# Kernel tuning notes

Hardware: AMD Instinct MI355X
Metric: run time of the kernel (lower is better)

The kernel has to match this reference:

```python
import jax, jax.numpy as jnp
import numpy as np

N = 262144      # total tokens (rows of batch)
D = 256         # d_model
S = 512         # number of distinct sequence ids
MAX_LEN = 640   # static upper bound on tokens per sequence (counts ~ Binomial(N, 1/S))


def setup_inputs() -> dict:
    key = jax.random.key(0)
    k1, k2 = jax.random.split(key)
    batch = jax.random.normal(k1, (N, D), dtype=jnp.float32)
    sequence_ids = jax.random.randint(k2, (N,), 0, S, dtype=jnp.int32)
    return {"batch": batch, "sequence_ids": sequence_ids}


def reference(batch, sequence_ids):
    # Counting-sort style grouping: for each row, compute its rank within its
    # sequence-id group (preserving original order, like torch.nonzero order),
    # then scatter into a padded [S, MAX_LEN, D] tensor.
    ids = sequence_ids
    ones = jnp.ones((N,), jnp.int32)
    counts = jax.ops.segment_sum(ones, ids, num_segments=S)          # [S]
    offsets = jnp.cumsum(counts) - counts                             # start of each group in sorted order
    order = jnp.argsort(ids)                                          # stable sort by id -> original order within group
    ranks_sorted = jnp.arange(N, dtype=jnp.int32) - offsets[ids[order]]
    ranks = jnp.zeros((N,), jnp.int32).at[order].set(ranks_sorted)    # rank of each row within its group
    padded = jnp.zeros((S, MAX_LEN, D), batch.dtype).at[ids, ranks].set(batch)
    padding_mask = jnp.all(padded == 0, axis=-1)                      # [S, MAX_LEN]
    return padded, padding_mask
```

## Files before the change

kernel.cpp:

```cpp
#include <hip/hip_runtime.h>

#define N_TOK   262144
#define D       256
#define NSEQ    512
#define MAX_LEN 640

#define CHUNK   256
#define NBLK    (N_TOK / CHUNK)
#define SEG     16
#define NSEGS   (NBLK / SEG)

__global__ __launch_bounds__(256) void k_hist(const int* __restrict__ ids,
                                              int* __restrict__ counts) {
    __shared__ int h[NSEQ];
    const int b = blockIdx.x;
    for (int i = threadIdx.x; i < NSEQ; i += 256) h[i] = 0;
    __syncthreads();
    const int id = ids[b * CHUNK + threadIdx.x];
    atomicAdd(&h[id], 1);
    __syncthreads();
    for (int i = threadIdx.x; i < NSEQ; i += 256) counts[b * NSEQ + i] = h[i];
}

__global__ __launch_bounds__(512) void k_segsum(const int* __restrict__ counts,
                                                int* __restrict__ segsum) {
    const int seg = blockIdx.x;
    const int s   = threadIdx.x;
    int acc = 0;
#pragma unroll
    for (int k = 0; k < SEG; ++k) acc += counts[(seg * SEG + k) * NSEQ + s];
    segsum[seg * NSEQ + s] = acc;
}

__global__ __launch_bounds__(512) void k_segscan(const int* __restrict__ segsum,
                                                 int* __restrict__ segpre,
                                                 int* __restrict__ totals) {
    const int s = threadIdx.x;
    int acc = 0;
    for (int g = 0; g < NSEGS; ++g) {
        segpre[g * NSEQ + s] = acc;
        acc += segsum[g * NSEQ + s];
    }
    totals[s] = acc;
}

__global__ __launch_bounds__(512) void k_expand(const int* __restrict__ counts,
                                                const int* __restrict__ segpre,
                                                int* __restrict__ prefix) {
    const int seg = blockIdx.x;
    const int s   = threadIdx.x;
    int acc = segpre[seg * NSEQ + s];
#pragma unroll
    for (int k = 0; k < SEG; ++k) {
        const int b = seg * SEG + k;
        prefix[b * NSEQ + s] = acc;
        acc += counts[b * NSEQ + s];
    }
}

__global__ __launch_bounds__(256) void k_scatter(const float* __restrict__ batch,
                                                 const int* __restrict__ ids,
                                                 const int* __restrict__ prefix,
                                                 float* __restrict__ padded) {
    __shared__ int lid[CHUNK];
    __shared__ int pre[NSEQ];
    __shared__ int drow[CHUNK];
    const int b = blockIdx.x;
    const int t = threadIdx.x;

    lid[t]       = ids[b * CHUNK + t];
    pre[t]       = prefix[b * NSEQ + t];
    pre[t + 256] = prefix[b * NSEQ + t + 256];
    __syncthreads();

    const int myid = lid[t];
    int r = 0;
    for (int j = 0; j < t; ++j) r += (lid[j] == myid);
    r += pre[myid];
    drow[t] = (r < MAX_LEN) ? (myid * MAX_LEN + r) : -1;
    __syncthreads();

    const int wave = t >> 6;
    const int lane = t & 63;
#pragma unroll 4
    for (int r2 = 0; r2 < 64; ++r2) {
        const int row = wave * 64 + r2;
        const int dr  = drow[row];
        if (dr < 0) continue;
        const float4* src = (const float4*)(batch + (size_t)(b * CHUNK + row) * D);
        float4*       dst = (float4*)(padded + (size_t)dr * D);
        dst[lane] = src[lane];
    }
}

__global__ __launch_bounds__(256) void k_zero(const int* __restrict__ totals,
                                              float* __restrict__ padded) {
    const int wid  = (blockIdx.x * 256 + threadIdx.x) >> 6;
    const int lane = threadIdx.x & 63;
    const int nw   = (gridDim.x * 256) >> 6;
    const float4 z = make_float4(0.f, 0.f, 0.f, 0.f);
    for (int slot = wid; slot < NSEQ * MAX_LEN; slot += nw) {
        const int s = slot / MAX_LEN;
        const int l = slot - s * MAX_LEN;
        if (l >= totals[s]) {
            ((float4*)(padded + (size_t)slot * D))[lane] = z;
        }
    }
}

__global__ __launch_bounds__(256) void k_mask(const int* __restrict__ totals,
                                              float* __restrict__ mask) {
    const int t = blockIdx.x * 256 + threadIdx.x;
    if (t >= NSEQ * MAX_LEN) return;
    const int s = t / MAX_LEN;
    const int l = t - s * MAX_LEN;
    mask[t] = (l >= totals[s]) ? 1.0f : 0.0f;
}

extern "C" void kernel_launch(void* const* d_in, const int* in_sizes, int n_in,
                              void* d_out, int out_size, void* d_ws, size_t ws_size,
                              hipStream_t stream) {
    const float* batch = (const float*)d_in[0];
    const int*   ids   = (const int*)d_in[1];

    float* padded = (float*)d_out;
    float* mask   = padded + (size_t)NSEQ * MAX_LEN * D;

    int* ws      = (int*)d_ws;
    int* counts  = ws;
    int* prefix  = counts + NBLK * NSEQ;
    int* segsum  = prefix + NBLK * NSEQ;
    int* segpre  = segsum + NSEGS * NSEQ;
    int* totals  = segpre + NSEGS * NSEQ;

    k_hist   <<<NBLK,  256, 0, stream>>>(ids, counts);
    k_segsum <<<NSEGS, 512, 0, stream>>>(counts, segsum);
    k_segscan<<<1,     512, 0, stream>>>(segsum, segpre, totals);
    k_expand <<<NSEGS, 512, 0, stream>>>(counts, segpre, prefix);
    k_scatter<<<NBLK,  256, 0, stream>>>(batch, ids, prefix, padded);
    k_zero   <<<2048,  256, 0, stream>>>(totals, padded);
    k_mask   <<<(NSEQ * MAX_LEN + 255) / 256, 256, 0, stream>>>(totals, mask);
}
```

Baseline: 156.4 us.

## Fuse counting, scan, scatter, zero-fill and mask kernels into three launches

Merges the per-chunk histogram with the segment sum, replaces the single-block serial segment scan with a redundant per-block prefix over earlier segments, and folds zero-fill and mask generation into the scatter kernel as extra blocks, one per sequence. The goal is to cut seven launches to three and remove the serial scan and the grid-stride zero pass that read totals for every slot. The scatter loop now issues its loads before the drop check and unrolls deeper to raise memory-level parallelism. In exchange, each zero-fill block does a serial loop over its sequence's padding rows, and blocks in the expand kernel do varying amounts of redundant summation.

```diff
diff --git a/kernel.cpp b/kernel.cpp
--- a/kernel.cpp
+++ b/kernel.cpp
@@ -10,111 +10,99 @@
 #define SEG     16
 #define NSEGS   (NBLK / SEG)
 
-__global__ __launch_bounds__(256) void k_hist(const int* __restrict__ ids,
-                                              int* __restrict__ counts) {
-    __shared__ int h[NSEQ];
-    const int b = blockIdx.x;
-    for (int i = threadIdx.x; i < NSEQ; i += 256) h[i] = 0;
+__global__ __launch_bounds__(512) void k_count(const int* __restrict__ ids,
+                                               int* __restrict__ counts,
+                                               int* __restrict__ segsum) {
+    __shared__ int h[SEG][NSEQ];
+    const int seg = blockIdx.x;
+    const int t   = threadIdx.x;
+#pragma unroll
+    for (int k = 0; k < SEG; ++k) h[k][t] = 0;
     __syncthreads();
-    const int id = ids[b * CHUNK + threadIdx.x];
-    atomicAdd(&h[id], 1);
+    const int base = seg * (SEG * CHUNK);
+#pragma unroll
+    for (int k = 0; k < 8; ++k) {
+        const int i  = t + 512 * k;
+        const int id = ids[base + i];
+        atomicAdd(&h[i >> 8][id], 1);
+    }
     __syncthreads();
-    for (int i = threadIdx.x; i < NSEQ; i += 256) counts[b * NSEQ + i] = h[i];
+    int acc = 0;
+#pragma unroll
+    for (int k = 0; k < SEG; ++k) {
+        const int c = h[k][t];
+        counts[(seg * SEG + k) * NSEQ + t] = c;
+        acc += c;
+    }
+    segsum[seg * NSEQ + t] = acc;
 }
 
-__global__ __launch_bounds__(512) void k_segsum(const int* __restrict__ counts,
-                                                int* __restrict__ segsum) {
+__global__ __launch_bounds__(512) void k_expand2(const int* __restrict__ counts,
+                                                 const int* __restrict__ segsum,
+                                                 int* __restrict__ prefix,
+                                                 int* __restrict__ totals) {
     const int seg = blockIdx.x;
-    const int s   = threadIdx.x;
+    const int t   = threadIdx.x;
     int acc = 0;
-#pragma unroll
-    for (int k = 0; k < SEG; ++k) acc += counts[(seg * SEG + k) * NSEQ + s];
-    segsum[seg * NSEQ + s] = acc;
-}
-
-__global__ __launch_bounds__(512) void k_segscan(const int* __restrict__ segsum,
-                                                 int* __restrict__ segpre,
-                                                 int* __restrict__ totals) {
-    const int s = threadIdx.x;
-    int acc = 0;
-    for (int g = 0; g < NSEGS; ++g) {
-        segpre[g * NSEQ + s] = acc;
-        acc += segsum[g * NSEQ + s];
-    }
-    totals[s] = acc;
-}
-
-__global__ __launch_bounds__(512) void k_expand(const int* __restrict__ counts,
-                                                const int* __restrict__ segpre,
-                                                int* __restrict__ prefix) {
-    const int seg = blockIdx.x;
-    const int s   = threadIdx.x;
-    int acc = segpre[seg * NSEQ + s];
+    for (int g = 0; g < seg; ++g) acc += segsum[g * NSEQ + t];
 #pragma unroll
     for (int k = 0; k < SEG; ++k) {
         const int b = seg * SEG + k;
-        prefix[b * NSEQ + s] = acc;
-        acc += counts[b * NSEQ + s];
+        prefix[b * NSEQ + t] = acc;
+        acc += counts[b * NSEQ + t];
     }
+    if (seg == NSEGS - 1) totals[t] = acc;
 }
 
-__global__ __launch_bounds__(256) void k_scatter(const float* __restrict__ batch,
-                                                 const int* __restrict__ ids,
-                                                 const int* __restrict__ prefix,
-                                                 float* __restrict__ padded) {
-    __shared__ int lid[CHUNK];
-    __shared__ int pre[NSEQ];
-    __shared__ int drow[CHUNK];
-    const int b = blockIdx.x;
+__global__ __launch_bounds__(256) void k_scatter_zero(const float* __restrict__ batch,
+                                                      const int* __restrict__ ids,
+                                                      const int* __restrict__ prefix,
+                                                      const int* __restrict__ totals,
+                                                      float* __restrict__ padded,
+                                                      float* __restrict__ mask) {
     const int t = threadIdx.x;
+    if (blockIdx.x < NBLK) {
+        __shared__ int lid[CHUNK];
+        __shared__ int pre[NSEQ];
+        __shared__ int drow[CHUNK];
+        const int b = blockIdx.x;
 
-    lid[t]       = ids[b * CHUNK + t];
-    pre[t]       = prefix[b * NSEQ + t];
-    pre[t + 256] = prefix[b * NSEQ + t + 256];
-    __syncthreads();
+        lid[t]       = ids[b * CHUNK + t];
+        pre[t]       = prefix[b * NSEQ + t];
+        pre[t + 256] = prefix[b * NSEQ + t + 256];
+        __syncthreads();
 
-    const int myid = lid[t];
-    int r = 0;
-    for (int j = 0; j < t; ++j) r += (lid[j] == myid);
-    r += pre[myid];
-    drow[t] = (r < MAX_LEN) ? (myid * MAX_LEN + r) : -1;
-    __syncthreads();
+        const int myid = lid[t];
+        int r = 0;
+        for (int j = 0; j < t; ++j) r += (lid[j] == myid);
+        r += pre[myid];
+        drow[t] = (r < MAX_LEN) ? (myid * MAX_LEN + r) : -1;
+        __syncthreads();
 
-    const int wave = t >> 6;
-    const int lane = t & 63;
-#pragma unroll 4
-    for (int r2 = 0; r2 < 64; ++r2) {
-        const int row = wave * 64 + r2;
-        const int dr  = drow[row];
-        if (dr < 0) continue;
-        const float4* src = (const float4*)(batch + (size_t)(b * CHUNK + row) * D);
-        float4*       dst = (float4*)(padded + (size_t)dr * D);
-        dst[lane] = src[lane];
-    }
-}
-
-__global__ __launch_bounds__(256) void k_zero(const int* __restrict__ totals,
-                                              float* __restrict__ padded) {
-    const int wid  = (blockIdx.x * 256 + threadIdx.x) >> 6;
-    const int lane = threadIdx.x & 63;
-    const int nw   = (gridDim.x * 256) >> 6;
-    const float4 z = make_float4(0.f, 0.f, 0.f, 0.f);
-    for (int slot = wid; slot < NSEQ * MAX_LEN; slot += nw) {
-        const int s = slot / MAX_LEN;
-        const int l = slot - s * MAX_LEN;
-        if (l >= totals[s]) {
-            ((float4*)(padded + (size_t)slot * D))[lane] = z;
+        const int wave = t >> 6;
+        const int lane = t & 63;
+#pragma unroll 8
+        for (int r2 = 0; r2 < 64; ++r2) {
+            const int row = wave * 64 + r2;
+            const float4 v =
+                ((const float4*)(batch + (size_t)(b * CHUNK + row) * D))[lane];
+            const int dr = drow[row];
+            if (dr >= 0)
+                ((float4*)(padded + (size_t)dr * D))[lane] = v;
+        }
+    } else {
+        const int s   = blockIdx.x - NBLK;
+        const int tot = totals[s];
+        const int wave = t >> 6;
+        const int lane = t & 63;
+        const float4 z = make_float4(0.f, 0.f, 0.f, 0.f);
+        for (int l = tot + wave; l < MAX_LEN; l += 4) {
+            ((float4*)(padded + (size_t)(s * MAX_LEN + l) * D))[lane] = z;
+        }
+        for (int l = t; l < MAX_LEN; l += 256) {
+            mask[s * MAX_LEN + l] = (l >= tot) ? 1.0f : 0.0f;
         }
     }
-}
-
-__global__ __launch_bounds__(256) void k_mask(const int* __restrict__ totals,
-                                              float* __restrict__ mask) {
-    const int t = blockIdx.x * 256 + threadIdx.x;
-    if (t >= NSEQ * MAX_LEN) return;
-    const int s = t / MAX_LEN;
-    const int l = t - s * MAX_LEN;
-    mask[t] = (l >= totals[s]) ? 1.0f : 0.0f;
 }
 
 extern "C" void kernel_launch(void* const* d_in, const int* in_sizes, int n_in,
@@ -126,18 +114,14 @@
     float* padded = (float*)d_out;
     float* mask   = padded + (size_t)NSEQ * MAX_LEN * D;
 
-    int* ws      = (int*)d_ws;
-    int* counts  = ws;
-    int* prefix  = counts + NBLK * NSEQ;
-    int* segsum  = prefix + NBLK * NSEQ;
-    int* segpre  = segsum + NSEGS * NSEQ;
-    int* totals  = segpre + NSEGS * NSEQ;
+    int* ws     = (int*)d_ws;
+    int* counts = ws;
+    int* prefix = counts + NBLK * NSEQ;
+    int* segsum = prefix + NBLK * NSEQ;
+    int* totals = segsum + NSEGS * NSEQ;
 
-    k_hist   <<<NBLK,  256, 0, stream>>>(ids, counts);
-    k_segsum <<<NSEGS, 512, 0, stream>>>(counts, segsum);
-    k_segscan<<<1,     512, 0, stream>>>(segsum, segpre, totals);
-    k_expand <<<NSEGS, 512, 0, stream>>>(counts, segpre, prefix);
-    k_scatter<<<NBLK,  256, 0, stream>>>(batch, ids, prefix, padded);
-    k_zero   <<<2048,  256, 0, stream>>>(totals, padded);
-    k_mask   <<<(NSEQ * MAX_LEN + 255) / 256, 256, 0, stream>>>(totals, mask);
+    k_count      <<<NSEGS,       512, 0, stream>>>(ids, counts, segsum);
+    k_expand2    <<<NSEGS,       512, 0, stream>>>(counts, segsum, prefix, totals);
+    k_scatter_zero<<<NBLK + NSEQ, 256, 0, stream>>>(batch, ids, prefix, totals,
+                                                    padded, mask);
 }
```

New measurement: 155.3 us. Within noise of the previous version (-0.7%).
